# Optimization experiments

Hardware: AMD Instinct MI355X
Metric: run time of the kernel (lower is better)

Reference implementation:

```python
import jax, jax.numpy as jnp
import numpy as np


def setup_inputs() -> dict:
    key = jax.random.key(0)
    ks = jax.random.split(key, 5)
    B, D, U = 16384, 512, 512
    return {
        "inputs": jax.random.normal(ks[0], (B, D), dtype=jnp.float32),
        "h_prev": jax.random.normal(ks[1], (B, U), dtype=jnp.float32),
        "update_kernel": jax.random.normal(ks[2], (D + U, U), dtype=jnp.float32) * 0.03,
        "reset_kernel": jax.random.normal(ks[3], (D + U, U), dtype=jnp.float32) * 0.03,
        "hidden_kernel": jax.random.normal(ks[4], (D + U, U), dtype=jnp.float32) * 0.03,
        "update_bias": jnp.zeros((U,), dtype=jnp.float32),
        "reset_bias": jnp.zeros((U,), dtype=jnp.float32),
        "hidden_bias": jnp.zeros((U,), dtype=jnp.float32),
    }


def reference(inputs, h_prev, update_kernel, reset_kernel, hidden_kernel,
              update_bias, reset_bias, hidden_bias):
    # fused_input: [B, D+U]
    fused = jnp.concatenate([inputs, h_prev], axis=-1)
    zg = jax.nn.sigmoid(fused @ update_kernel + update_bias)   # update gate [B,U]
    rg = jax.nn.sigmoid(fused @ reset_kernel + reset_bias)     # reset gate  [B,U]
    h_tilde = jnp.tanh(
        jnp.concatenate([inputs, rg * h_prev], axis=-1) @ hidden_kernel + hidden_bias
    )
    ht = (1.0 - zg) * h_prev + zg * h_tilde
    return ht
```

## Files before the change

### kernel.cpp

```cpp
#include <hip/hip_runtime.h>
#include <hip/hip_bf16.h>
#include <math.h>

typedef __attribute__((ext_vector_type(4))) float f32x4;
typedef __attribute__((ext_vector_type(8))) float f32x8;
typedef __bf16 bf16x8 __attribute__((ext_vector_type(8)));
typedef unsigned short u16;
typedef u16 u16x8 __attribute__((ext_vector_type(8)));
typedef void __attribute__((address_space(1))) * as1p;
typedef void __attribute__((address_space(3))) * as3p;

#define WAITVM8() asm volatile("s_waitcnt vmcnt(8)" ::: "memory")
#define WAITVM4() asm volatile("s_waitcnt vmcnt(4)" ::: "memory")
#define WAITVM0() asm volatile("s_waitcnt vmcnt(0)" ::: "memory")
#define SBAR()    __builtin_amdgcn_s_barrier()
#define SCHEDB()  __builtin_amdgcn_sched_barrier(0)

__device__ __forceinline__ unsigned short f2bf(float f) {
    union { float f; unsigned int u; } v; v.f = f;
    unsigned int u = v.u;
    u += 0x7fffu + ((u >> 16) & 1u);
    return (unsigned short)(u >> 16);
}

__device__ __forceinline__ float bf2f(unsigned short b) {
    union { unsigned int u; float f; } v;
    v.u = ((unsigned int)b) << 16;
    return v.f;
}

__device__ __forceinline__ float fast_tanh(float v) {
    float vc = fminf(fmaxf(v, -15.f), 15.f);
    float e = __expf(2.f * vc);
    return (e - 1.f) / (e + 1.f);
}

__global__ void prep_k(const float* __restrict__ x, const float* __restrict__ h,
                       const float* __restrict__ wz, const float* __restrict__ wrr,
                       const float* __restrict__ wh,
                       u16* __restrict__ xb, u16* __restrict__ hb,
                       u16* __restrict__ wzt, u16* __restrict__ wrt, u16* __restrict__ wht) {
    __shared__ float t[32][33];
    int bid = blockIdx.x;
    int tid = threadIdx.x;
    if (bid < 2048) {
        const int n4 = 16384 * 512 / 4;
        int i = bid * 256 + tid;
        const int stride = 2048 * 256;
        const float4* x4 = (const float4*)x;
        const float4* h4 = (const float4*)h;
        ushort4* xb4 = (ushort4*)xb;
        ushort4* hb4 = (ushort4*)hb;
        for (; i < n4; i += stride) {
            float4 v = x4[i];
            xb4[i] = make_ushort4(f2bf(v.x), f2bf(v.y), f2bf(v.z), f2bf(v.w));
            float4 w = h4[i];
            hb4[i] = make_ushort4(f2bf(w.x), f2bf(w.y), f2bf(w.z), f2bf(w.w));
        }
    } else {
        int b = bid - 2048;
        int z = b >> 9;
        int rem = b & 511;
        const float* src = (z == 0) ? wz : (z == 1) ? wrr : wh;
        u16* dst = (z == 0) ? wzt : (z == 1) ? wrt : wht;
        int n0 = (rem & 15) * 32;
        int k0 = (rem >> 4) * 32;
        int tx = tid & 31, ty = tid >> 5;
#pragma unroll
        for (int i = 0; i < 4; ++i)
            t[ty + i * 8][tx] = src[(size_t)(k0 + ty + i * 8) * 512 + n0 + tx];
        __syncthreads();
#pragma unroll
        for (int i = 0; i < 4; ++i)
            dst[(size_t)(n0 + ty + i * 8) * 1024 + k0 + tx] = f2bf(t[tx][ty + i * 8]);
    }
}

__device__ __forceinline__ void stage32(const u16* g, int gstride, u16* region, int tid) {
#pragma unroll
    for (int i = 0; i < 2; ++i) {
        int ob = i * 4096 + ((tid >> 6) << 10);
        int o = ob + ((tid & 63) << 4);
        int row = o >> 6;
        int cb = (o & 63) ^ ((row & 3) << 4);
        const u16* gp = g + (size_t)row * gstride + (cb >> 1);
        __builtin_amdgcn_global_load_lds((as1p)(void*)gp, (as3p)(void*)(region + (ob >> 1)), 16, 0, 0);
    }
}

__device__ __forceinline__ bf16x8 ld32(const u16* region, int r, int kb) {
    int byte = (r << 6) + (kb ^ ((r & 3) << 4));
    return *(const bf16x8*)((const char*)region + byte);
}

__device__ __forceinline__ void compute32(const u16* LA, const u16* LB,
                                          int wr, int wc, int l, f32x4 (&acc)[4][4]) {
    int fr = l & 15;
    int kbb = (l >> 4) << 4;
    bf16x8 a[4], b[4];
#pragma unroll
    for (int m = 0; m < 4; ++m)
        a[m] = ld32(LA, wr * 64 + m * 16 + fr, kbb);
#pragma unroll
    for (int n = 0; n < 4; ++n)
        b[n] = ld32(LB, wc * 64 + n * 16 + fr, kbb);
#pragma unroll
    for (int m = 0; m < 4; ++m)
#pragma unroll
        for (int n = 0; n < 4; ++n)
            acc[m][n] = __builtin_amdgcn_mfma_f32_16x16x32_bf16(a[m], b[n], acc[m][n], 0, 0, 0);
}

template<typename AF, typename BF>
__device__ __forceinline__ void kring(AF ga, BF gb, u16* lds, int tid,
                                      int wr, int wc, int l, f32x4 (&acc)[4][4]) {
#pragma unroll
    for (int t = 0; t < 3; ++t) {
        u16* b = lds + t * 8192;
        stage32(ga(t), 512, b, tid);
        stage32(gb(t), 1024, b + 4096, tid);
    }
#pragma unroll
    for (int i = 0; i < 29; ++i) {
        WAITVM8(); SCHEDB();
        SBAR(); SCHEDB();
        u16* nb_ = lds + ((i + 3) & 3) * 8192;
        stage32(ga(i + 3), 512, nb_, tid);
        stage32(gb(i + 3), 1024, nb_ + 4096, tid);
        const u16* cur = lds + (i & 3) * 8192;
        compute32(cur, cur + 4096, wr, wc, l, acc);
    }
    WAITVM8(); SCHEDB(); SBAR(); SCHEDB();
    { const u16* cur = lds + (29 & 3) * 8192; compute32(cur, cur + 4096, wr, wc, l, acc); }
    WAITVM4(); SCHEDB(); SBAR(); SCHEDB();
    { const u16* cur = lds + (30 & 3) * 8192; compute32(cur, cur + 4096, wr, wc, l, acc); }
    WAITVM0(); SCHEDB(); SBAR(); SCHEDB();
    { const u16* cur = lds + (31 & 3) * 8192; compute32(cur, cur + 4096, wr, wc, l, acc); }
}

__device__ __forceinline__ void scatter_half(float* tf, const f32x4 (&acc)[4][4],
                                             int wc, int l) {
    int colb = wc * 64;
    int rowb = (l >> 4) << 2;
#pragma unroll
    for (int n = 0; n < 4; ++n) {
        int col = colb + n * 16 + (l & 15);
#pragma unroll
        for (int m = 0; m < 4; ++m) {
            int row0 = rowb + m * 16;
#pragma unroll
            for (int r = 0; r < 4; ++r)
                tf[(row0 + r) * 128 + col] = acc[m][n][r];
        }
    }
}

__global__ __launch_bounds__(256, 2) void zr_k(
    const u16* __restrict__ Xb, const u16* __restrict__ Hb,
    const u16* __restrict__ Wzt, const u16* __restrict__ Wrt,
    const float* __restrict__ ub, const float* __restrict__ rb_,
    u16* __restrict__ zgb, u16* __restrict__ rgh) {
    __shared__ u16 lds[4 * 8192];
    int tid = threadIdx.x;
    int l = tid & 63, w = tid >> 6;
    int wr = w >> 1, wc = w & 1;
    int swz = (blockIdx.x & 7) * 128 + (blockIdx.x >> 3);
    int mb = swz >> 3, nb = swz & 7;
    int m0 = mb * 128, n0 = nb * 128;
    bool isZ = (n0 < 512);
    const u16* Wt = isZ ? Wzt : Wrt;
    int nw = isZ ? n0 : (n0 - 512);

    f32x4 acc[4][4];
#pragma unroll
    for (int m = 0; m < 4; ++m)
#pragma unroll
        for (int n = 0; n < 4; ++n) acc[m][n] = (f32x4){0.f, 0.f, 0.f, 0.f};

    auto ga = [&](int t) -> const u16* {
        return (t < 16) ? (Xb + (size_t)m0 * 512 + t * 32)
                        : (Hb + (size_t)m0 * 512 + (t - 16) * 32);
    };
    auto gb = [&](int t) -> const u16* { return Wt + (size_t)nw * 1024 + t * 32; };
    kring(ga, gb, lds, tid, wr, wc, l, acc);

    float* tf = (float*)lds;
#pragma unroll
    for (int half = 0; half < 2; ++half) {
        __syncthreads();
        if (wr == half) scatter_half(tf, acc, wc, l);
        __syncthreads();
#pragma unroll
        for (int it = 0; it < 4; ++it) {
            int chunk = it * 256 + tid;
            int row = chunk >> 4;
            int c8 = (chunk & 15) << 3;
            f32x8 v8 = *(const f32x8*)&tf[row * 128 + c8];
            int gcol = nw + c8;
            size_t gbase = (size_t)(m0 + half * 64 + row) * 512 + gcol;
            if (isZ) {
                f32x8 bv = *(const f32x8*)&ub[gcol];
                u16x8 o;
#pragma unroll
                for (int j = 0; j < 8; ++j)
                    o[j] = f2bf(1.f / (1.f + __expf(-(v8[j] + bv[j]))));
                *(u16x8*)&zgb[gbase] = o;
            } else {
                f32x8 bv = *(const f32x8*)&rb_[gcol];
                u16x8 h8 = *(const u16x8*)&Hb[gbase];
                u16x8 o;
#pragma unroll
                for (int j = 0; j < 8; ++j) {
                    float s = 1.f / (1.f + __expf(-(v8[j] + bv[j])));
                    o[j] = f2bf(s * bf2f(h8[j]));
                }
                *(u16x8*)&rgh[gbase] = o;
            }
        }
    }
}

__global__ __launch_bounds__(256, 2) void gh_k(
    const u16* __restrict__ Xb, const u16* __restrict__ rgh, const u16* __restrict__ Wt,
    const float* __restrict__ hp, const u16* __restrict__ zgb, const float* __restrict__ hb,
    float* __restrict__ out) {
    __shared__ u16 lds[4 * 8192];
    int tid = threadIdx.x;
    int l = tid & 63, w = tid >> 6;
    int wr = w >> 1, wc = w & 1;
    int swz = (blockIdx.x & 7) * 64 + (blockIdx.x >> 3);
    int mb = swz >> 2, nb = swz & 3;
    int m0 = mb * 128, n0 = nb * 128;
    f32x4 acc[4][4];
#pragma unroll
    for (int m = 0; m < 4; ++m)
#pragma unroll
        for (int n = 0; n < 4; ++n) acc[m][n] = (f32x4){0.f, 0.f, 0.f, 0.f};

    auto ga = [&](int t) -> const u16* {
        return (t < 16) ? (Xb + (size_t)m0 * 512 + t * 32)
                        : (rgh + (size_t)m0 * 512 + (t - 16) * 32);
    };
    auto gb = [&](int t) -> const u16* { return Wt + (size_t)n0 * 1024 + t * 32; };
    kring(ga, gb, lds, tid, wr, wc, l, acc);

    float* tf = (float*)lds;
#pragma unroll
    for (int half = 0; half < 2; ++half) {
        __syncthreads();
        if (wr == half) scatter_half(tf, acc, wc, l);
        __syncthreads();
#pragma unroll
        for (int it = 0; it < 4; ++it) {
            int chunk = it * 256 + tid;
            int row = chunk >> 4;
            int c8 = (chunk & 15) << 3;
            f32x8 v8 = *(const f32x8*)&tf[row * 128 + c8];
            int gcol = n0 + c8;
            size_t gbase = (size_t)(m0 + half * 64 + row) * 512 + gcol;
            f32x8 hbv = *(const f32x8*)&hb[gcol];
            f32x8 h8 = *(const f32x8*)&hp[gbase];
            u16x8 z8 = *(const u16x8*)&zgb[gbase];
            f32x8 o;
#pragma unroll
            for (int j = 0; j < 8; ++j) {
                float t = fast_tanh(v8[j] + hbv[j]);
                float z = bf2f(z8[j]);
                o[j] = h8[j] + z * (t - h8[j]);
            }
            *(f32x8*)&out[gbase] = o;
        }
    }
}

extern "C" void kernel_launch(void* const* d_in, const int* in_sizes, int n_in,
                              void* d_out, int out_size, void* d_ws, size_t ws_size,
                              hipStream_t stream) {
    const float* x  = (const float*)d_in[0];
    const float* h  = (const float*)d_in[1];
    const float* wz = (const float*)d_in[2];
    const float* wr = (const float*)d_in[3];
    const float* wh = (const float*)d_in[4];
    const float* ub = (const float*)d_in[5];
    const float* rb = (const float*)d_in[6];
    const float* hb = (const float*)d_in[7];
    float* out = (float*)d_out;

    const int B = 16384;
    char* ws = (char*)d_ws;
    size_t off = 0;
    u16* Xb  = (u16*)(ws + off); off += (size_t)B * 512 * 2;
    u16* Hb  = (u16*)(ws + off); off += (size_t)B * 512 * 2;
    u16* Wzt = (u16*)(ws + off); off += (size_t)512 * 1024 * 2;
    u16* Wrt = (u16*)(ws + off); off += (size_t)512 * 1024 * 2;
    u16* Wht = (u16*)(ws + off); off += (size_t)512 * 1024 * 2;
    u16* rgh = (u16*)(ws + off); off += (size_t)B * 512 * 2;
    u16* zgb = (u16*)(ws + off); off += (size_t)B * 512 * 2;

    prep_k<<<2048 + 1536, 256, 0, stream>>>(x, h, wz, wr, wh, Xb, Hb, Wzt, Wrt, Wht);

    zr_k<<<1024, 256, 0, stream>>>(Xb, Hb, Wzt, Wrt, ub, rb, zgb, rgh);
    gh_k<<<512, 256, 0, stream>>>(Xb, rgh, Wht, h, zgb, hb, out);
}
```

Baseline: 98.66 us.

## Switch GEMMs to 256x256 tiles with 8-wave ping-pong pipeline and K=64 stages

Replaces the 128x128-tile, 4-wave GEMM with a 256x256-tile, 8-wave kernel that uses 128 KB of dynamic LDS. The K loop is now double-buffered in 64-wide steps with an 8-row XOR swizzle, and staging is interleaved between quarter-tile MFMA groups separated by barriers and s_setprio. The aim is more operand reuse per LDS byte and more overlap of global loads with matrix math. In exchange, gemm1 launches only 256 blocks and gemm2 only 128, one block per CU, which risks leaving many of the mi355x's CUs idle and adds many block-wide barriers.

```diff
diff --git a/kernel.cpp b/kernel.cpp
--- a/kernel.cpp
+++ b/kernel.cpp
@@ -10,11 +10,10 @@
 typedef void __attribute__((address_space(1))) * as1p;
 typedef void __attribute__((address_space(3))) * as3p;
 
-#define WAITVM8() asm volatile("s_waitcnt vmcnt(8)" ::: "memory")
-#define WAITVM4() asm volatile("s_waitcnt vmcnt(4)" ::: "memory")
-#define WAITVM0() asm volatile("s_waitcnt vmcnt(0)" ::: "memory")
-#define SBAR()    __builtin_amdgcn_s_barrier()
-#define SCHEDB()  __builtin_amdgcn_sched_barrier(0)
+#define SCHEDB() __builtin_amdgcn_sched_barrier(0)
+#define BAR()    __builtin_amdgcn_s_barrier()
+#define VM4()    asm volatile("s_waitcnt vmcnt(4)" ::: "memory")
+#define VM0()    asm volatile("s_waitcnt vmcnt(0)" ::: "memory")
 
 __device__ __forceinline__ unsigned short f2bf(float f) {
     union { float f; unsigned int u; } v; v.f = f;
@@ -76,128 +75,194 @@
     }
 }
 
-__device__ __forceinline__ void stage32(const u16* g, int gstride, u16* region, int tid) {
-#pragma unroll
-    for (int i = 0; i < 2; ++i) {
-        int ob = i * 4096 + ((tid >> 6) << 10);
+#define RGN(L, b, r) ((L) + (b) * 32768 + (r) * 8192)
+
+__device__ __forceinline__ void stage_half512(const u16* g, int gstride, u16* region, int tid) {
+#pragma unroll
+    for (int rd = 0; rd < 2; ++rd) {
+        int ob = rd * 8192 + ((tid >> 6) << 10);
         int o = ob + ((tid & 63) << 4);
-        int row = o >> 6;
-        int cb = (o & 63) ^ ((row & 3) << 4);
+        int row = o >> 7;
+        int cb = (o & 127) ^ ((row & 7) << 4);
         const u16* gp = g + (size_t)row * gstride + (cb >> 1);
         __builtin_amdgcn_global_load_lds((as1p)(void*)gp, (as3p)(void*)(region + (ob >> 1)), 16, 0, 0);
     }
 }
 
-__device__ __forceinline__ bf16x8 ld32(const u16* region, int r, int kb) {
-    int byte = (r << 6) + (kb ^ ((r & 3) << 4));
+__device__ __forceinline__ bf16x8 ld_frag(const u16* region, int r, int kb) {
+    int byte = (r << 7) + (kb ^ ((r & 7) << 4));
     return *(const bf16x8*)((const char*)region + byte);
 }
 
-__device__ __forceinline__ void compute32(const u16* LA, const u16* LB,
-                                          int wr, int wc, int l, f32x4 (&acc)[4][4]) {
-    int fr = l & 15;
-    int kbb = (l >> 4) << 4;
-    bf16x8 a[4], b[4];
-#pragma unroll
-    for (int m = 0; m < 4; ++m)
-        a[m] = ld32(LA, wr * 64 + m * 16 + fr, kbb);
-#pragma unroll
-    for (int n = 0; n < 4; ++n)
-        b[n] = ld32(LB, wc * 64 + n * 16 + fr, kbb);
-#pragma unroll
-    for (int m = 0; m < 4; ++m)
-#pragma unroll
-        for (int n = 0; n < 4; ++n)
-            acc[m][n] = __builtin_amdgcn_mfma_f32_16x16x32_bf16(a[m], b[n], acc[m][n], 0, 0, 0);
-}
-
-template<typename AF, typename BF>
-__device__ __forceinline__ void kring(AF ga, BF gb, u16* lds, int tid,
-                                      int wr, int wc, int l, f32x4 (&acc)[4][4]) {
-#pragma unroll
-    for (int t = 0; t < 3; ++t) {
-        u16* b = lds + t * 8192;
-        stage32(ga(t), 512, b, tid);
-        stage32(gb(t), 1024, b + 4096, tid);
-    }
-#pragma unroll
-    for (int i = 0; i < 29; ++i) {
-        WAITVM8(); SCHEDB();
-        SBAR(); SCHEDB();
-        u16* nb_ = lds + ((i + 3) & 3) * 8192;
-        stage32(ga(i + 3), 512, nb_, tid);
-        stage32(gb(i + 3), 1024, nb_ + 4096, tid);
-        const u16* cur = lds + (i & 3) * 8192;
-        compute32(cur, cur + 4096, wr, wc, l, acc);
-    }
-    WAITVM8(); SCHEDB(); SBAR(); SCHEDB();
-    { const u16* cur = lds + (29 & 3) * 8192; compute32(cur, cur + 4096, wr, wc, l, acc); }
-    WAITVM4(); SCHEDB(); SBAR(); SCHEDB();
-    { const u16* cur = lds + (30 & 3) * 8192; compute32(cur, cur + 4096, wr, wc, l, acc); }
-    WAITVM0(); SCHEDB(); SBAR(); SCHEDB();
-    { const u16* cur = lds + (31 & 3) * 8192; compute32(cur, cur + 4096, wr, wc, l, acc); }
-}
-
-__device__ __forceinline__ void scatter_half(float* tf, const f32x4 (&acc)[4][4],
-                                             int wc, int l) {
-    int colb = wc * 64;
-    int rowb = (l >> 4) << 2;
-#pragma unroll
-    for (int n = 0; n < 4; ++n) {
-        int col = colb + n * 16 + (l & 15);
-#pragma unroll
-        for (int m = 0; m < 4; ++m) {
-            int row0 = rowb + m * 16;
-#pragma unroll
-            for (int r = 0; r < 4; ++r)
-                tf[(row0 + r) * 128 + col] = acc[m][n][r];
-        }
-    }
-}
-
-__global__ __launch_bounds__(256, 2) void zr_k(
+__device__ __forceinline__ void rdA(const u16* rg, int base_r, int kbb, bf16x8 (&a)[4][2]) {
+#pragma unroll
+    for (int mf = 0; mf < 4; ++mf)
+#pragma unroll
+        for (int q = 0; q < 2; ++q)
+            a[mf][q] = ld_frag(rg, base_r + mf * 16, q * 64 + kbb);
+}
+
+__device__ __forceinline__ void rdB(const u16* rg, int base_r, int kbb, bf16x8 (&b)[2][2]) {
+#pragma unroll
+    for (int nf = 0; nf < 2; ++nf)
+#pragma unroll
+        for (int q = 0; q < 2; ++q)
+            b[nf][q] = ld_frag(rg, base_r + nf * 16, q * 64 + kbb);
+}
+
+template<int MH, int NH>
+__device__ __forceinline__ void mm16(f32x4 (&acc)[8][4], const bf16x8 (&a)[4][2],
+                                     const bf16x8 (&b)[2][2]) {
+    __builtin_amdgcn_s_setprio(1);
+#pragma unroll
+    for (int q = 0; q < 2; ++q)
+#pragma unroll
+        for (int mf = 0; mf < 4; ++mf)
+#pragma unroll
+            for (int nf = 0; nf < 2; ++nf)
+                acc[MH * 4 + mf][NH * 2 + nf] = __builtin_amdgcn_mfma_f32_16x16x32_bf16(
+                    a[mf][q], b[nf][q], acc[MH * 4 + mf][NH * 2 + nf], 0, 0, 0);
+    __builtin_amdgcn_s_setprio(0);
+}
+
+__device__ __forceinline__ void core8(const u16* AX, const u16* AH, const u16* BW,
+                                      u16* lds, int tid, f32x4 (&acc)[8][4]) {
+    const int l = tid & 63, w = tid >> 6;
+    const int wr = w >> 2, wc = w & 3;
+    const int fr = l & 15, kbb = (l >> 4) << 4;
+    const int br0 = (wc & 1) * 64 + fr;
+
+    auto ap = [&](int t, int h) -> const u16* {
+        const u16* base = (t < 8) ? (AX + t * 64) : (AH + (t - 8) * 64);
+        return base + (size_t)h * (128 * 512);
+    };
+    auto bp = [&](int t, int h) -> const u16* {
+        return BW + (size_t)h * (128 * 1024) + t * 64;
+    };
+
+    stage_half512(bp(0, 0), 1024, RGN(lds, 0, 2), tid);
+    stage_half512(bp(0, 1), 1024, RGN(lds, 0, 3), tid);
+    stage_half512(ap(0, 0), 512,  RGN(lds, 0, 0), tid);
+    stage_half512(ap(0, 1), 512,  RGN(lds, 0, 1), tid);
+    stage_half512(bp(1, 0), 1024, RGN(lds, 1, 2), tid);
+    stage_half512(bp(1, 1), 1024, RGN(lds, 1, 3), tid);
+    VM4(); SCHEDB(); BAR();
+
+    bf16x8 a[4][2], b0[2][2], b1[2][2];
+
+    for (int t = 0; t < 14; ++t) {
+        const int bt = t & 1;
+        const u16* Ar = RGN(lds, bt, wr);
+        const u16* Br = RGN(lds, bt, 2 + (wc >> 1));
+        rdA(Ar, fr, kbb, a);
+        rdB(Br, br0, kbb, b0);
+        stage_half512(ap(t + 1, 0), 512, RGN(lds, 1 - bt, 0), tid);
+        BAR();
+        mm16<0, 0>(acc, a, b0);
+        BAR();
+        rdB(Br, br0 + 32, kbb, b1);
+        stage_half512(ap(t + 1, 1), 512, RGN(lds, 1 - bt, 1), tid);
+        BAR();
+        mm16<0, 1>(acc, a, b1);
+        BAR();
+        rdA(Ar, 64 + fr, kbb, a);
+        stage_half512(bp(t + 2, 0), 1024, RGN(lds, bt, 2), tid);
+        BAR();
+        mm16<1, 1>(acc, a, b1);
+        BAR();
+        stage_half512(bp(t + 2, 1), 1024, RGN(lds, bt, 3), tid);
+        BAR();
+        mm16<1, 0>(acc, a, b0);
+        VM4(); SCHEDB();
+        BAR();
+    }
+    {
+        const u16* Ar = RGN(lds, 0, wr);
+        const u16* Br = RGN(lds, 0, 2 + (wc >> 1));
+        rdA(Ar, fr, kbb, a); rdB(Br, br0, kbb, b0);
+        stage_half512(ap(15, 0), 512, RGN(lds, 1, 0), tid);
+        BAR(); mm16<0, 0>(acc, a, b0); BAR();
+        rdB(Br, br0 + 32, kbb, b1);
+        stage_half512(ap(15, 1), 512, RGN(lds, 1, 1), tid);
+        BAR(); mm16<0, 1>(acc, a, b1); BAR();
+        rdA(Ar, 64 + fr, kbb, a);
+        BAR(); mm16<1, 1>(acc, a, b1); BAR();
+        BAR(); mm16<1, 0>(acc, a, b0);
+        VM0(); SCHEDB();
+        BAR();
+    }
+    {
+        const u16* Ar = RGN(lds, 1, wr);
+        const u16* Br = RGN(lds, 1, 2 + (wc >> 1));
+        rdA(Ar, fr, kbb, a); rdB(Br, br0, kbb, b0);
+        BAR(); mm16<0, 0>(acc, a, b0); BAR();
+        rdB(Br, br0 + 32, kbb, b1);
+        BAR(); mm16<0, 1>(acc, a, b1); BAR();
+        rdA(Ar, 64 + fr, kbb, a);
+        BAR(); mm16<1, 1>(acc, a, b1); BAR();
+        BAR(); mm16<1, 0>(acc, a, b0);
+    }
+}
+
+__device__ __forceinline__ void scat(float* tf, const f32x4 (&acc)[8][4],
+                                     int wr, int wc, int l, int ch) {
+    if ((wc >> 1) != ch) return;
+    int rb = wr * 128 + ((l >> 4) << 2);
+    int cb = (wc & 1) * 64 + (l & 15);
+#pragma unroll
+    for (int mh = 0; mh < 2; ++mh)
+#pragma unroll
+        for (int mf = 0; mf < 4; ++mf)
+#pragma unroll
+            for (int nh = 0; nh < 2; ++nh)
+#pragma unroll
+                for (int nf = 0; nf < 2; ++nf) {
+                    int row = rb + mh * 64 + mf * 16;
+                    int col = cb + nh * 32 + nf * 16;
+#pragma unroll
+                    for (int r = 0; r < 4; ++r)
+                        tf[(row + r) * 128 + col] = acc[mh * 4 + mf][nh * 2 + nf][r];
+                }
+}
+
+__global__ __launch_bounds__(512, 1) void gemm1_k(
     const u16* __restrict__ Xb, const u16* __restrict__ Hb,
     const u16* __restrict__ Wzt, const u16* __restrict__ Wrt,
     const float* __restrict__ ub, const float* __restrict__ rb_,
     u16* __restrict__ zgb, u16* __restrict__ rgh) {
-    __shared__ u16 lds[4 * 8192];
-    int tid = threadIdx.x;
-    int l = tid & 63, w = tid >> 6;
-    int wr = w >> 1, wc = w & 1;
-    int swz = (blockIdx.x & 7) * 128 + (blockIdx.x >> 3);
-    int mb = swz >> 3, nb = swz & 7;
-    int m0 = mb * 128, n0 = nb * 128;
+    extern __shared__ u16 lds[];
+    const int tid = threadIdx.x;
+    const int l = tid & 63, w = tid >> 6, wr = w >> 2, wc = w & 3;
+    int swz = (blockIdx.x & 7) * 32 + (blockIdx.x >> 3);
+    int mb = swz >> 2, nb = swz & 3;
+    int m0 = mb * 256, n0 = nb * 256;
     bool isZ = (n0 < 512);
+    int cbase = isZ ? n0 : (n0 - 512);
     const u16* Wt = isZ ? Wzt : Wrt;
-    int nw = isZ ? n0 : (n0 - 512);
-
-    f32x4 acc[4][4];
-#pragma unroll
-    for (int m = 0; m < 4; ++m)
+
+    f32x4 acc[8][4];
+#pragma unroll
+    for (int m = 0; m < 8; ++m)
 #pragma unroll
         for (int n = 0; n < 4; ++n) acc[m][n] = (f32x4){0.f, 0.f, 0.f, 0.f};
 
-    auto ga = [&](int t) -> const u16* {
-        return (t < 16) ? (Xb + (size_t)m0 * 512 + t * 32)
-                        : (Hb + (size_t)m0 * 512 + (t - 16) * 32);
-    };
-    auto gb = [&](int t) -> const u16* { return Wt + (size_t)nw * 1024 + t * 32; };
-    kring(ga, gb, lds, tid, wr, wc, l, acc);
+    core8(Xb + (size_t)m0 * 512, Hb + (size_t)m0 * 512, Wt + (size_t)cbase * 1024,
+          lds, tid, acc);
 
     float* tf = (float*)lds;
 #pragma unroll
-    for (int half = 0; half < 2; ++half) {
-        __syncthreads();
-        if (wr == half) scatter_half(tf, acc, wc, l);
-        __syncthreads();
-#pragma unroll
-        for (int it = 0; it < 4; ++it) {
-            int chunk = it * 256 + tid;
+    for (int ch = 0; ch < 2; ++ch) {
+        __syncthreads();
+        scat(tf, acc, wr, wc, l, ch);
+        __syncthreads();
+#pragma unroll
+        for (int it = 0; it < 8; ++it) {
+            int chunk = it * 512 + tid;
             int row = chunk >> 4;
             int c8 = (chunk & 15) << 3;
             f32x8 v8 = *(const f32x8*)&tf[row * 128 + c8];
-            int gcol = nw + c8;
-            size_t gbase = (size_t)(m0 + half * 64 + row) * 512 + gcol;
+            int gcol = cbase + ch * 128 + c8;
+            size_t gbase = (size_t)(m0 + row) * 512 + gcol;
             if (isZ) {
                 f32x8 bv = *(const f32x8*)&ub[gcol];
                 u16x8 o;
@@ -220,51 +285,47 @@
     }
 }
 
-__global__ __launch_bounds__(256, 2) void gh_k(
-    const u16* __restrict__ Xb, const u16* __restrict__ rgh, const u16* __restrict__ Wt,
-    const float* __restrict__ hp, const u16* __restrict__ zgb, const float* __restrict__ hb,
+__global__ __launch_bounds__(512, 1) void gemm2_k(
+    const u16* __restrict__ Xb, const u16* __restrict__ rgh, const u16* __restrict__ Wht,
+    const float* __restrict__ hp, const u16* __restrict__ zgb, const float* __restrict__ hbv,
     float* __restrict__ out) {
-    __shared__ u16 lds[4 * 8192];
-    int tid = threadIdx.x;
-    int l = tid & 63, w = tid >> 6;
-    int wr = w >> 1, wc = w & 1;
-    int swz = (blockIdx.x & 7) * 64 + (blockIdx.x >> 3);
-    int mb = swz >> 2, nb = swz & 3;
-    int m0 = mb * 128, n0 = nb * 128;
-    f32x4 acc[4][4];
-#pragma unroll
-    for (int m = 0; m < 4; ++m)
+    extern __shared__ u16 lds[];
+    const int tid = threadIdx.x;
+    const int l = tid & 63, w = tid >> 6, wr = w >> 2, wc = w & 3;
+    int swz = (blockIdx.x & 7) * 16 + (blockIdx.x >> 3);
+    int mb = swz >> 1, nb = swz & 1;
+    int m0 = mb * 256, n0 = nb * 256;
+
+    f32x4 acc[8][4];
+#pragma unroll
+    for (int m = 0; m < 8; ++m)
 #pragma unroll
         for (int n = 0; n < 4; ++n) acc[m][n] = (f32x4){0.f, 0.f, 0.f, 0.f};
 
-    auto ga = [&](int t) -> const u16* {
-        return (t < 16) ? (Xb + (size_t)m0 * 512 + t * 32)
-                        : (rgh + (size_t)m0 * 512 + (t - 16) * 32);
-    };
-    auto gb = [&](int t) -> const u16* { return Wt + (size_t)n0 * 1024 + t * 32; };
-    kring(ga, gb, lds, tid, wr, wc, l, acc);
+    core8(Xb + (size_t)m0 * 512, rgh + (size_t)m0 * 512, Wht + (size_t)n0 * 1024,
+          lds, tid, acc);
 
     float* tf = (float*)lds;
 #pragma unroll
-    for (int half = 0; half < 2; ++half) {
-        __syncthreads();
-        if (wr == half) scatter_half(tf, acc, wc, l);
-        __syncthreads();
-#pragma unroll
-        for (int it = 0; it < 4; ++it) {
-            int chunk = it * 256 + tid;
+    for (int ch = 0; ch < 2; ++ch) {
+        __syncthreads();
+        scat(tf, acc, wr, wc, l, ch);
+        __syncthreads();
+#pragma unroll
+        for (int it = 0; it < 8; ++it) {
+            int chunk = it * 512 + tid;
             int row = chunk >> 4;
             int c8 = (chunk & 15) << 3;
             f32x8 v8 = *(const f32x8*)&tf[row * 128 + c8];
-            int gcol = n0 + c8;
-            size_t gbase = (size_t)(m0 + half * 64 + row) * 512 + gcol;
-            f32x8 hbv = *(const f32x8*)&hb[gcol];
+            int gcol = n0 + ch * 128 + c8;
+            size_t gbase = (size_t)(m0 + row) * 512 + gcol;
+            f32x8 bv = *(const f32x8*)&hbv[gcol];
             f32x8 h8 = *(const f32x8*)&hp[gbase];
             u16x8 z8 = *(const u16x8*)&zgb[gbase];
             f32x8 o;
 #pragma unroll
             for (int j = 0; j < 8; ++j) {
-                float t = fast_tanh(v8[j] + hbv[j]);
+                float t = fast_tanh(v8[j] + bv[j]);
                 float z = bf2f(z8[j]);
                 o[j] = h8[j] + z * (t - h8[j]);
             }
@@ -297,8 +358,11 @@
     u16* rgh = (u16*)(ws + off); off += (size_t)B * 512 * 2;
     u16* zgb = (u16*)(ws + off); off += (size_t)B * 512 * 2;
 
+    hipFuncSetAttribute((const void*)gemm1_k, hipFuncAttributeMaxDynamicSharedMemorySize, 131072);
+    hipFuncSetAttribute((const void*)gemm2_k, hipFuncAttributeMaxDynamicSharedMemorySize, 131072);
+
     prep_k<<<2048 + 1536, 256, 0, stream>>>(x, h, wz, wr, wh, Xb, Hb, Wzt, Wrt, Wht);
 
-    zr_k<<<1024, 256, 0, stream>>>(Xb, Hb, Wzt, Wrt, ub, rb, zgb, rgh);
-    gh_k<<<512, 256, 0, stream>>>(Xb, rgh, Wht, h, zgb, hb, out);
-}
+    gemm1_k<<<256, 512, 131072, stream>>>(Xb, Hb, Wzt, Wrt, ub, rb, zgb, rgh);
+    gemm2_k<<<128, 512, 131072, stream>>>(Xb, rgh, Wht, h, zgb, hb, out);
+}
```

New measurement: 104.9 us. 1.06x slower.
